# Optimization experiments

Hardware: AMD Instinct MI355X
Metric: run time of the kernel (lower is better)

The kernel has to match this reference:

```python
import jax, jax.numpy as jnp
import numpy as np

N = 1_000_000   # number of integration points
KAPPA = 100.0   # bulk modulus (init kwarg)
BETA = 2.0      # VolumetricPart.beta default


def det33(A):
    # closed-form determinant of batched 3x3 matrices [N,3,3]
    return (A[..., 0, 0] * (A[..., 1, 1] * A[..., 2, 2] - A[..., 1, 2] * A[..., 2, 1])
            - A[..., 0, 1] * (A[..., 1, 0] * A[..., 2, 2] - A[..., 1, 2] * A[..., 2, 0])
            + A[..., 0, 2] * (A[..., 1, 0] * A[..., 2, 1] - A[..., 1, 1] * A[..., 2, 0]))


def setup_inputs() -> dict:
    key = jax.random.key(0)
    kF, = jax.random.split(key, 1)
    # deformation gradient near identity so det(F) > 0 (valid kinematics)
    F = jnp.eye(3, dtype=jnp.float32) + 0.1 * jax.random.normal(kF, (N, 3, 3), dtype=jnp.float32)
    mu = jnp.array([0.63, 0.0012, -0.01], dtype=jnp.float32)   # Ogden shear moduli
    alpha = jnp.array([1.3, 5.0, -2.0], dtype=jnp.float32)     # Ogden exponents
    return {"F": F, "mu": mu, "alpha": alpha}


def reference(F, mu, alpha):
    # C = F^T F  -> [N,3,3] symmetric positive definite
    C = jnp.einsum('nki,nkj->nij', F, F)
    J = jnp.sqrt(det33(C))                      # [N]
    Cb = J[:, None, None] ** (-2.0 / 3.0) * C   # isochoric right Cauchy-Green
    lamb = jnp.linalg.eigvalsh(Cb)              # [N,3] eigenvalues (positive)
    alp2 = alpha * 0.5                          # [K]
    # sum_i lamb_i^(alpha_k/2) -> [N,K]
    pw = jnp.sum(lamb[:, :, None] ** alp2[None, None, :], axis=1)
    W_iso = jnp.sum((mu / alpha) * (pw - 3.0), axis=-1)        # [N]
    W_vol = KAPPA * (1.0 / (BETA * BETA)) * (J ** BETA - BETA * jnp.log(J) - 1.0)
    return W_iso + W_vol                        # [N] strain energy per point
```

## Files before the change

### kernel.cpp

```cpp
#include <hip/hip_runtime.h>


#define BLOCK 256
#define LN2F 0.6931471805599453f

__device__ __forceinline__ float fast_acos(float x) {
    const float ax = fabsf(x);
    const float t  = __builtin_amdgcn_sqrtf(1.0f - ax);
    const float p  = 1.5707288f + ax * (-0.2121144f + ax * (0.0742610f - ax * 0.0187293f));
    const float ac = t * p;
    return (x >= 0.0f) ? ac : (3.14159265358979f - ac);
}

__global__ __launch_bounds__(BLOCK) void ogden_kernel(
    const float* __restrict__ F,
    const float* __restrict__ mu,
    const float* __restrict__ alpha,
    float* __restrict__ out, int n)
{
    __shared__ float sF[BLOCK * 9];

    const int tid  = threadIdx.x;
    const int base = blockIdx.x * BLOCK;

    long long gbase = (long long)base * 9;
    int limit = (n - base) * 9;
    if (limit > BLOCK * 9) limit = BLOCK * 9;
    #pragma unroll
    for (int j = 0; j < 9; ++j) {
        int idx = j * BLOCK + tid;
        if (idx < limit) sF[idx] = F[gbase + idx];
    }
    __syncthreads();

    const int i = base + tid;
    if (i >= n) return;

    const float* f = &sF[tid * 9];
    const float f00 = f[0], f01 = f[1], f02 = f[2];
    const float f10 = f[3], f11 = f[4], f12 = f[5];
    const float f20 = f[6], f21 = f[7], f22 = f[8];

    const float c00 = f00*f00 + f10*f10 + f20*f20;
    const float c01 = f00*f01 + f10*f11 + f20*f21;
    const float c02 = f00*f02 + f10*f12 + f20*f22;
    const float c11 = f01*f01 + f11*f11 + f21*f21;
    const float c12 = f01*f02 + f11*f12 + f21*f22;
    const float c22 = f02*f02 + f12*f12 + f22*f22;

    const float detF = f00*(f11*f22 - f12*f21)
                     - f01*(f10*f22 - f12*f20)
                     + f02*(f10*f21 - f11*f20);
    const float J     = fabsf(detF);
    const float log2J = __builtin_amdgcn_logf(J);
    const float lnJ   = log2J * LN2F;

    const float s = __builtin_amdgcn_exp2f(-(2.0f/3.0f) * log2J);
    const float b00 = s*c00, b01 = s*c01, b02 = s*c02;
    const float b11 = s*c11, b12 = s*c12, b22 = s*c22;

    const float q  = (b00 + b11 + b22) * (1.0f/3.0f);
    const float d0 = b00 - q, d1 = b11 - q, d2 = b22 - q;
    const float p2 = d0*d0 + d1*d1 + d2*d2
                   + 2.0f*(b01*b01 + b02*b02 + b12*b12);
    const float p  = __builtin_amdgcn_sqrtf(p2 * (1.0f/6.0f));
    const float invp = (p > 1e-20f) ? __builtin_amdgcn_rcpf(p) : 0.0f;

    const float m00 = d0*invp, m01 = b01*invp, m02 = b02*invp;
    const float m11 = d1*invp, m12 = b12*invp, m22 = d2*invp;
    const float detB = m00*(m11*m22 - m12*m12)
                     - m01*(m01*m22 - m12*m02)
                     + m02*(m01*m12 - m11*m02);
    float r = 0.5f * detB;
    r = fminf(1.0f, fmaxf(-1.0f, r));

    const float phi  = fast_acos(r) * (1.0f/3.0f);
    const float twop = 2.0f * p;
    float l1 = q + twop * __cosf(phi);
    float l3 = q + twop * __cosf(phi + 2.0943951023931953f);
    float l2 = 3.0f*q - l1 - l3;

    l1 = fmaxf(l1, 1e-12f);
    l2 = fmaxf(l2, 1e-12f);
    l3 = fmaxf(l3, 1e-12f);

    const float lg1 = __builtin_amdgcn_logf(l1);
    const float lg2 = __builtin_amdgcn_logf(l2);
    const float lg3 = __builtin_amdgcn_logf(l3);

    float W = 0.0f;
    #pragma unroll
    for (int k = 0; k < 3; ++k) {
        const float ak = alpha[k];
        const float a2 = 0.5f * ak;
        const float pw = __builtin_amdgcn_exp2f(a2 * lg1)
                       + __builtin_amdgcn_exp2f(a2 * lg2)
                       + __builtin_amdgcn_exp2f(a2 * lg3);
        W += (mu[k] / ak) * (pw - 3.0f);
    }

    W += 25.0f * (J*J - 2.0f*lnJ - 1.0f);

    out[i] = W;
}

extern "C" void kernel_launch(void* const* d_in, const int* in_sizes, int n_in,
                              void* d_out, int out_size, void* d_ws, size_t ws_size,
                              hipStream_t stream) {
    const float* F     = (const float*)d_in[0];
    const float* mu    = (const float*)d_in[1];
    const float* alpha = (const float*)d_in[2];
    float* out = (float*)d_out;
    const int n = out_size;

    const int grid = (n + BLOCK - 1) / BLOCK;
    ogden_kernel<<<grid, BLOCK, 0, stream>>>(F, mu, alpha, out, n);
}
```

Before: 83.24 us.

## Process two points per thread with float4 LDS staging and algebraic simplifications

Each thread now handles two integration points, and the block stages twice as many deformation gradients into shared memory using float4 loads. The eigen solve runs on C directly, with the isochoric scaling applied as a log-domain shift, and the third eigenvalue's log is taken as minus the sum of the other two. The mu/alpha ratios are computed once per thread instead of inside the per-point loop. The aim is fewer, wider global loads, fewer transcendental calls and more work per thread, at the cost of doubled LDS use per block, which may lower occupancy. Using the fast rcp for mu/alpha also adds a small precision risk.

```diff
diff --git a/kernel.cpp b/kernel.cpp
--- a/kernel.cpp
+++ b/kernel.cpp
@@ -2,6 +2,10 @@
 
 
 #define BLOCK 256
+#define PPT 2
+#define PTS (BLOCK * PPT)
+#define LDS_FLOATS (PTS * 9)
+#define LDS_VEC4 (LDS_FLOATS / 4)
 #define LN2F 0.6931471805599453f
 
 __device__ __forceinline__ float fast_acos(float x) {
@@ -12,31 +16,11 @@
     return (x >= 0.0f) ? ac : (3.14159265358979f - ac);
 }
 
-__global__ __launch_bounds__(BLOCK) void ogden_kernel(
-    const float* __restrict__ F,
-    const float* __restrict__ mu,
-    const float* __restrict__ alpha,
-    float* __restrict__ out, int n)
+__device__ __forceinline__ float ogden_point(
+    const float* __restrict__ f,
+    float h0, float h1, float h2,
+    float ma0, float ma1, float ma2)
 {
-    __shared__ float sF[BLOCK * 9];
-
-    const int tid  = threadIdx.x;
-    const int base = blockIdx.x * BLOCK;
-
-    long long gbase = (long long)base * 9;
-    int limit = (n - base) * 9;
-    if (limit > BLOCK * 9) limit = BLOCK * 9;
-    #pragma unroll
-    for (int j = 0; j < 9; ++j) {
-        int idx = j * BLOCK + tid;
-        if (idx < limit) sF[idx] = F[gbase + idx];
-    }
-    __syncthreads();
-
-    const int i = base + tid;
-    if (i >= n) return;
-
-    const float* f = &sF[tid * 9];
     const float f00 = f[0], f01 = f[1], f02 = f[2];
     const float f10 = f[3], f11 = f[4], f12 = f[5];
     const float f20 = f[6], f21 = f[7], f22 = f[8];
@@ -53,21 +37,16 @@
                      + f02*(f10*f21 - f11*f20);
     const float J     = fabsf(detF);
     const float log2J = __builtin_amdgcn_logf(J);
-    const float lnJ   = log2J * LN2F;
 
-    const float s = __builtin_amdgcn_exp2f(-(2.0f/3.0f) * log2J);
-    const float b00 = s*c00, b01 = s*c01, b02 = s*c02;
-    const float b11 = s*c11, b12 = s*c12, b22 = s*c22;
-
-    const float q  = (b00 + b11 + b22) * (1.0f/3.0f);
-    const float d0 = b00 - q, d1 = b11 - q, d2 = b22 - q;
+    const float q  = (c00 + c11 + c22) * (1.0f/3.0f);
+    const float d0 = c00 - q, d1 = c11 - q, d2 = c22 - q;
     const float p2 = d0*d0 + d1*d1 + d2*d2
-                   + 2.0f*(b01*b01 + b02*b02 + b12*b12);
-    const float p  = __builtin_amdgcn_sqrtf(p2 * (1.0f/6.0f));
+                   + 2.0f*(c01*c01 + c02*c02 + c12*c12);
+    const float p    = __builtin_amdgcn_sqrtf(p2 * (1.0f/6.0f));
     const float invp = (p > 1e-20f) ? __builtin_amdgcn_rcpf(p) : 0.0f;
 
-    const float m00 = d0*invp, m01 = b01*invp, m02 = b02*invp;
-    const float m11 = d1*invp, m12 = b12*invp, m22 = d2*invp;
+    const float m00 = d0*invp, m01 = c01*invp, m02 = c02*invp;
+    const float m11 = d1*invp, m12 = c12*invp, m22 = d2*invp;
     const float detB = m00*(m11*m22 - m12*m12)
                      - m01*(m01*m22 - m12*m02)
                      + m02*(m01*m12 - m11*m02);
@@ -78,30 +57,67 @@
     const float twop = 2.0f * p;
     float l1 = q + twop * __cosf(phi);
     float l3 = q + twop * __cosf(phi + 2.0943951023931953f);
-    float l2 = 3.0f*q - l1 - l3;
 
     l1 = fmaxf(l1, 1e-12f);
-    l2 = fmaxf(l2, 1e-12f);
     l3 = fmaxf(l3, 1e-12f);
 
-    const float lg1 = __builtin_amdgcn_logf(l1);
-    const float lg2 = __builtin_amdgcn_logf(l2);
-    const float lg3 = __builtin_amdgcn_logf(l3);
+    const float shift = -(2.0f/3.0f) * log2J;
+    const float t1 = __builtin_amdgcn_logf(l1) + shift;
+    const float t3 = __builtin_amdgcn_logf(l3) + shift;
+    const float t2 = -(t1 + t3);
 
-    float W = 0.0f;
+    const float pw0 = __builtin_amdgcn_exp2f(h0*t1)
+                    + __builtin_amdgcn_exp2f(h0*t2)
+                    + __builtin_amdgcn_exp2f(h0*t3);
+    const float pw1 = __builtin_amdgcn_exp2f(h1*t1)
+                    + __builtin_amdgcn_exp2f(h1*t2)
+                    + __builtin_amdgcn_exp2f(h1*t3);
+    const float pw2 = __builtin_amdgcn_exp2f(h2*t1)
+                    + __builtin_amdgcn_exp2f(h2*t2)
+                    + __builtin_amdgcn_exp2f(h2*t3);
+    float W = ma0*(pw0 - 3.0f) + ma1*(pw1 - 3.0f) + ma2*(pw2 - 3.0f);
+
+    W += 25.0f * (J*J - 2.0f*(log2J*LN2F) - 1.0f);
+    return W;
+}
+
+__global__ __launch_bounds__(BLOCK) void ogden_kernel(
+    const float* __restrict__ F,
+    const float* __restrict__ mu,
+    const float* __restrict__ alpha,
+    float* __restrict__ out, int n)
+{
+    __shared__ float sF[LDS_FLOATS];
+
+    const int tid  = threadIdx.x;
+    const int base = blockIdx.x * PTS;
+
+    int nf = (n - base) * 9;
+    if (nf > LDS_FLOATS) nf = LDS_FLOATS;
+    const int nf4 = nf >> 2;
+    const float4* __restrict__ G4 = (const float4*)(F + (long long)base * 9);
+    float4* S4 = (float4*)sF;
     #pragma unroll
-    for (int k = 0; k < 3; ++k) {
-        const float ak = alpha[k];
-        const float a2 = 0.5f * ak;
-        const float pw = __builtin_amdgcn_exp2f(a2 * lg1)
-                       + __builtin_amdgcn_exp2f(a2 * lg2)
-                       + __builtin_amdgcn_exp2f(a2 * lg3);
-        W += (mu[k] / ak) * (pw - 3.0f);
+    for (int j = 0; j < LDS_VEC4 / BLOCK + 1; ++j) {
+        const int idx = j * BLOCK + tid;
+        if (idx < nf4) S4[idx] = G4[idx];
     }
+    const int rem = nf & 3;
+    if (tid < rem) sF[nf4 * 4 + tid] = F[(long long)base * 9 + nf4 * 4 + tid];
+    __syncthreads();
 
-    W += 25.0f * (J*J - 2.0f*lnJ - 1.0f);
+    const float a0 = alpha[0], a1 = alpha[1], a2 = alpha[2];
+    const float h0 = 0.5f * a0, h1 = 0.5f * a1, h2 = 0.5f * a2;
+    const float ma0 = mu[0] * __builtin_amdgcn_rcpf(a0);
+    const float ma1 = mu[1] * __builtin_amdgcn_rcpf(a1);
+    const float ma2 = mu[2] * __builtin_amdgcn_rcpf(a2);
 
-    out[i] = W;
+    const float W0 = ogden_point(&sF[tid * 9],           h0, h1, h2, ma0, ma1, ma2);
+    const float W1 = ogden_point(&sF[(tid + BLOCK) * 9], h0, h1, h2, ma0, ma1, ma2);
+
+    const int i0 = base + tid;
+    if (i0 < n)         out[i0]         = W0;
+    if (i0 + BLOCK < n) out[i0 + BLOCK] = W1;
 }
 
 extern "C" void kernel_launch(void* const* d_in, const int* in_sizes, int n_in,
@@ -113,6 +129,6 @@
     float* out = (float*)d_out;
     const int n = out_size;
 
-    const int grid = (n + BLOCK - 1) / BLOCK;
+    const int grid = (n + PTS - 1) / PTS;
     ogden_kernel<<<grid, BLOCK, 0, stream>>>(F, mu, alpha, out, n);
 }
```

Result: no change. 82.34 us (-1.1%).
